# Kernel tuning notes

Hardware: AMD Instinct MI355X
Metric: run time of the kernel (lower is better)

Reference implementation:

```python
import jax, jax.numpy as jnp
import numpy as np

NUM_ITERATIONS = 5
BIG = 1e30


def _compute_cv(vc, Hf, norm):
    # vc: [B, M, N]; Hf: [M, N] float 0/1 mask; norm: scalar normalization factor
    # sign part: product of signs of incoming messages per check, redistributed
    sign_info = (1.0 - Hf)[None] + vc            # non-edges -> +1 so they don't affect the product
    s = jnp.sign(sign_info)
    row_sign = jnp.prod(s, axis=2, keepdims=True)  # [B, M, 1]
    result_sign = row_sign * Hf * s              # extrinsic sign per edge (self sign divided out)
    # magnitude part: min / second-min over edges of each check (masked top-2)
    back = jnp.where(Hf == 0.0, -BIG - 1.0, 0.0)[None]  # push non-edges to -inf-ish
    a = jnp.clip(jnp.abs(vc), 0.0, BIG)
    decision = -a + back                          # top-2 of this = two smallest magnitudes on edges
    top2 = jax.lax.top_k(decision, 2)[0]          # [B, M, 2]
    mn = (-top2[:, :, 0:1]) * Hf                  # smallest magnitude, broadcast on edges
    sub = (-top2[:, :, 1:2]) * Hf                 # second smallest
    res = jnp.where(a > mn, mn, sub)              # extrinsic min (exclude self if self is the min)
    return norm * res * jax.lax.stop_gradient(result_sign)


def setup_inputs() -> dict:
    key = jax.random.key(0)
    k1, k2, k3 = jax.random.split(key, 3)
    B, M, N = 16, 1024, 2048
    soft_input = jax.random.normal(k1, (B, N), dtype=jnp.float32) * 2.0
    # sparse binary parity-check matrix (Tanner graph), ~20 ones per row, min degree 2
    H = (jax.random.uniform(k2, (M, N)) < 0.01).astype(jnp.int32)
    H = H.at[:, :2].set(1)
    labels = jax.random.randint(k3, (B, N), 0, 2).astype(jnp.int32)
    w = jnp.full((1,), -0.048, dtype=jnp.float32)
    return {"soft_input": soft_input, "H": H, "labels": labels, "w": w}


def reference(soft_input, H, labels, w):
    Hf = H.astype(jnp.float32)
    norm = jax.nn.softplus(w)  # NMS-1 normalized factor, shape [1]
    soft_output = soft_input
    for _ in range(NUM_ITERATIONS):
        vc = soft_output[:, None, :] * Hf          # variable-to-check messages [B, M, N]
        cv = _compute_cv(vc, Hf, norm)             # check-to-variable messages [B, M, N]
        soft_output = soft_input + jnp.sum(cv, axis=1)  # marginalize
    return soft_output
```

## Files before the change

kernel.cpp:

```cpp
#include <hip/hip_runtime.h>

#define BB 16
#define MM 1024
#define NN 2048
#define RCAP 64
#define CCAP 48
#define NBLK 256
#define NTHR 1024
#define GRP  16
#define CPB  (NN / GRP)
#define INFF __builtin_inff()

typedef unsigned short u16;

__device__ __forceinline__ float signf(float x) {
    return (x > 0.0f) ? 1.0f : ((x < 0.0f) ? -1.0f : 0.0f);
}

__device__ __forceinline__ float loadB(const float* p) {
    unsigned u = __hip_atomic_load((const unsigned*)p, __ATOMIC_RELAXED,
                                   __HIP_MEMORY_SCOPE_AGENT);
    return __uint_as_float(u);
}
__device__ __forceinline__ void storeB(float* p, float v) {
    __hip_atomic_store((unsigned*)p, __float_as_uint(v), __ATOMIC_RELAXED,
                       __HIP_MEMORY_SCOPE_AGENT);
}

__device__ __forceinline__ void bar_global(int* c) {
    asm volatile("s_waitcnt vmcnt(0)" ::: "memory");
    __syncthreads();
    if (threadIdx.x == 0) {
        __hip_atomic_fetch_add(c, 1, __ATOMIC_ACQ_REL, __HIP_MEMORY_SCOPE_AGENT);
        while (__hip_atomic_load(c, __ATOMIC_RELAXED, __HIP_MEMORY_SCOPE_AGENT) < NBLK)
            __builtin_amdgcn_s_sleep(1);
        (void)__hip_atomic_load(c, __ATOMIC_ACQUIRE, __HIP_MEMORY_SCOPE_AGENT);
    }
    __syncthreads();
}

__device__ __forceinline__ void bar_group(int* c) {
    asm volatile("s_waitcnt vmcnt(0)" ::: "memory");
    __syncthreads();
    if (threadIdx.x == 0) {
        __hip_atomic_fetch_add(c, 1, __ATOMIC_RELAXED, __HIP_MEMORY_SCOPE_AGENT);
        while (__hip_atomic_load(c, __ATOMIC_RELAXED, __HIP_MEMORY_SCOPE_AGENT) < GRP)
            __builtin_amdgcn_s_sleep(1);
    }
    __syncthreads();
}

__global__ __launch_bounds__(NTHR)
void bp_one(const int4* __restrict__ H4, const float* __restrict__ soft_in,
            const float* __restrict__ wptr,
            int* __restrict__ ctrG, int* __restrict__ ctr2,
            int* __restrict__ col_deg, int* __restrict__ row_deg,
            u16* __restrict__ row_cols, u16* __restrict__ col_rows,
            float* __restrict__ sX, float* __restrict__ sY,
            float* __restrict__ out)
{
    __shared__ float  s_soft[NN];
    __shared__ float4 s_stats[MM];
    __shared__ u16    s_deg[MM];
    __shared__ u16    s_cols[4][RCAP];
    __shared__ int    s_cnt[4];

    const int t = threadIdx.x;

    if (t < 4) s_cnt[t] = 0;
    __syncthreads();
    const int lr = t >> 8;
    const int tt = t & 255;
    const int mrow = blockIdx.x * 4 + lr;
    {
        const int4* hrow = H4 + mrow * (NN / 4);
#pragma unroll
        for (int h = 0; h < 2; ++h) {
            int i = tt + (h << 8);
            int4 hv4 = hrow[i];
            int hv[4] = {hv4.x, hv4.y, hv4.z, hv4.w};
#pragma unroll
            for (int kk = 0; kk < 4; ++kk) {
                if (hv[kk]) {
                    int j = atomicAdd(&s_cnt[lr], 1);
                    if (j < RCAP) s_cols[lr][j] = (u16)(i * 4 + kk);
                }
            }
        }
    }
    __syncthreads();
    const int rdeg_local = min(s_cnt[lr], RCAP);
    if (tt == 0) row_deg[mrow] = rdeg_local;
    if (tt < 8) ((int4*)(row_cols + mrow * RCAP))[tt] = ((const int4*)s_cols[lr])[tt];
    if (tt < rdeg_local) {
        int c = s_cols[lr][tt];
        if (c >= 2) {
            int pos = atomicAdd(&col_deg[c], 1);
            if (pos < CCAP) col_rows[c * CCAP + pos] = (u16)mrow;
        }
    }
    bar_global(ctrG);

    const int g    = blockIdx.x & 15;
    const int rank = blockIdx.x >> 4;
    const float norm = log1pf(expf(wptr[0]));
    const float* sInG = soft_in + g * NN;
    float* sXg = sX + g * NN;
    float* sYg = sY + g * NN;
    float* outG = out + g * NN;

    s_deg[t] = (u16)row_deg[t];

    const int myCol = rank * CPB + (t >> 3);
    const int ll = t & 7;
    const int cdeg = (myCol >= 2) ? min(col_deg[myCol], CCAP) : 0;
    const bool cact = (ll < 6) && ((ll << 3) < cdeg);
    int4 ci = make_int4(0, 0, 0, 0);
    if (cact) ci = ((const int4*)(col_rows + myCol * CCAP))[ll];
    const float x_in_col = sInG[myCol];
    const bool heavy = (rank == 0) && (t < 128);
    const int hc = t >> 6;
    const float x_in_h = heavy ? sInG[hc] : 0.0f;
    __syncthreads();

#pragma unroll 1
    for (int it = 0; it < 5; ++it) {
        const float* curG = (it & 1) ? sXg : sYg;
        float* nxtG = (it & 1) ? sYg : sXg;

        {
            float v0, v1;
            if (it == 0) { v0 = sInG[t]; v1 = sInG[t + 1024]; }
            else         { v0 = loadB(curG + t); v1 = loadB(curG + t + 1024); }
            s_soft[t] = v0; s_soft[t + 1024] = v1;
        }
        __syncthreads();

        {
            const int deg = s_deg[t];
            const int4* ip = (const int4*)(row_cols + t * RCAP);
            float sgn = 1.0f, mn = INFF, sub = INFF;
#pragma unroll
            for (int jb = 0; jb < RCAP; jb += 8) {
                if (jb < deg) {
                    int4 iv = ip[jb >> 3];
                    const u16* q = (const u16*)&iv;
#pragma unroll
                    for (int k = 0; k < 8; ++k) {
                        float x = s_soft[q[k] & (NN - 1)];
                        x = (jb + k < deg) ? x : INFF;
                        sgn *= signf(x);
                        float a = fabsf(x);
                        if (a < mn) { sub = mn; mn = a; }
                        else if (a < sub) sub = a;
                    }
                }
            }
            s_stats[t] = make_float4(norm * sgn, mn, sub, 0.0f);
        }
        __syncthreads();

        float res;
        {
            float x = s_soft[myCol];
            float a = fabsf(x), sx = signf(x), acc = 0.0f;
            if (cact) {
                const u16* q = (const u16*)&ci;
                const int base = ll << 3;
#pragma unroll
                for (int k = 0; k < 8; ++k) {
                    float4 s = s_stats[q[k] & (MM - 1)];
                    float cv = s.x * ((a > s.y) ? s.y : s.z) * sx;
                    acc += (base + k < cdeg) ? cv : 0.0f;
                }
            }
            acc += __shfl_xor(acc, 1);
            acc += __shfl_xor(acc, 2);
            acc += __shfl_xor(acc, 4);
            res = x_in_col + acc;
        }
        float hres = 0.0f;
        if (heavy) {
            const int lane = t & 63;
            float x = s_soft[hc];
            float a = fabsf(x), sx = signf(x), acc = 0.0f;
#pragma unroll
            for (int i2 = 0; i2 < 16; ++i2) {
                float4 s = s_stats[lane + (i2 << 6)];
                acc += s.x * ((a > s.y) ? s.y : s.z) * sx;
            }
#pragma unroll
            for (int off = 1; off < 64; off <<= 1) acc += __shfl_xor(acc, off);
            hres = x_in_h + acc;
        }

        const bool writer = (ll == 0) && (myCol >= 2);
        const bool hwriter = heavy && ((t & 63) == 0);
        if (it < 4) {
            if (writer)  storeB(nxtG + myCol, res);
            if (hwriter) storeB(nxtG + hc, hres);
            bar_group(ctr2 + ((g << 2) + it) * 64);
        } else {
            if (writer)  outG[myCol] = res;
            if (hwriter) outG[hc] = hres;
        }
    }
}

extern "C" void kernel_launch(void* const* d_in, const int* in_sizes, int n_in,
                              void* d_out, int out_size, void* d_ws, size_t ws_size,
                              hipStream_t stream)
{
    const float* soft_in = (const float*)d_in[0];
    const int4*  H4      = (const int4*)d_in[1];
    const float* w       = (const float*)d_in[3];
    float* out = (float*)d_out;

    char* ws = (char*)d_ws;
    int* ctrG     = (int*)ws;
    int* ctr2     = (int*)(ws + 1024);
    int* col_deg  = (int*)(ws + 20480);
    int* row_deg  = (int*)(ws + 28672);
    u16* row_cols = (u16*)(ws + 32768);
    u16* col_rows = (u16*)(ws + 163840);
    float* sX     = (float*)(ws + 360448);
    float* sY     = (float*)(ws + 491520);

    hipMemsetAsync(ws, 0, 28672, stream);

    void* args[12] = { (void*)&H4, (void*)&soft_in, (void*)&w,
                       (void*)&ctrG, (void*)&ctr2, (void*)&col_deg,
                       (void*)&row_deg, (void*)&row_cols, (void*)&col_rows,
                       (void*)&sX, (void*)&sY, (void*)&out };
    hipLaunchCooperativeKernel((void*)bp_one, dim3(NBLK), dim3(NTHR),
                               args, 0, stream);
}
```

Before: 147.7 us.

## Replace counter barriers with flag barriers and vectorize inter-block exchange

```diff
diff --git a/kernel.cpp b/kernel.cpp
--- a/kernel.cpp
+++ b/kernel.cpp
@@ -12,66 +12,91 @@
 #define INFF __builtin_inff()
 
 typedef unsigned short u16;
+typedef unsigned int u32;
+typedef float f32x4 __attribute__((ext_vector_type(4)));
 
 __device__ __forceinline__ float signf(float x) {
     return (x > 0.0f) ? 1.0f : ((x < 0.0f) ? -1.0f : 0.0f);
 }
 
-__device__ __forceinline__ float loadB(const float* p) {
-    unsigned u = __hip_atomic_load((const unsigned*)p, __ATOMIC_RELAXED,
-                                   __HIP_MEMORY_SCOPE_AGENT);
-    return __uint_as_float(u);
-}
-__device__ __forceinline__ void storeB(float* p, float v) {
-    __hip_atomic_store((unsigned*)p, __float_as_uint(v), __ATOMIC_RELAXED,
-                       __HIP_MEMORY_SCOPE_AGENT);
-}
-
-__device__ __forceinline__ void bar_global(int* c) {
+__device__ __forceinline__ f32x4 loadB4(const float* p) {
+    f32x4 v;
+    asm volatile("global_load_dwordx4 %0, %1, off sc0 sc1\n\t"
+                 "s_waitcnt vmcnt(0)"
+                 : "=&v"(v) : "v"(p) : "memory");
+    return v;
+}
+__device__ __forceinline__ void storeB4(float* p, f32x4 v) {
+    asm volatile("global_store_dwordx4 %0, %1, off sc0 sc1"
+                 :: "v"(p), "v"(v) : "memory");
+}
+__device__ __forceinline__ int loadBi(const int* p) {
+    return __hip_atomic_load(p, __ATOMIC_RELAXED, __HIP_MEMORY_SCOPE_AGENT);
+}
+
+__device__ __forceinline__ void bar_build(int* bf) {
     asm volatile("s_waitcnt vmcnt(0)" ::: "memory");
     __syncthreads();
-    if (threadIdx.x == 0) {
-        __hip_atomic_fetch_add(c, 1, __ATOMIC_ACQ_REL, __HIP_MEMORY_SCOPE_AGENT);
-        while (__hip_atomic_load(c, __ATOMIC_RELAXED, __HIP_MEMORY_SCOPE_AGENT) < NBLK)
-            __builtin_amdgcn_s_sleep(1);
-        (void)__hip_atomic_load(c, __ATOMIC_ACQUIRE, __HIP_MEMORY_SCOPE_AGENT);
-    }
-    __syncthreads();
-}
-
-__device__ __forceinline__ void bar_group(int* c) {
+    if (threadIdx.x == 0)
+        __hip_atomic_store(bf + blockIdx.x, 1, __ATOMIC_RELEASE,
+                           __HIP_MEMORY_SCOPE_AGENT);
+    if (threadIdx.x < 64) {
+        const int i = (int)threadIdx.x << 2;
+        for (;;) {
+            int a = loadBi(bf + i) & loadBi(bf + i + 1) &
+                    loadBi(bf + i + 2) & loadBi(bf + i + 3);
+            if (__all(a)) break;
+            __builtin_amdgcn_s_sleep(8);
+        }
+    }
+    __syncthreads();
+    if (threadIdx.x == 0)
+        (void)__hip_atomic_load(bf, __ATOMIC_ACQUIRE, __HIP_MEMORY_SCOPE_AGENT);
+    __syncthreads();
+}
+
+__device__ __forceinline__ void bar_group(int* gf, int rank, int target) {
     asm volatile("s_waitcnt vmcnt(0)" ::: "memory");
     __syncthreads();
-    if (threadIdx.x == 0) {
-        __hip_atomic_fetch_add(c, 1, __ATOMIC_RELAXED, __HIP_MEMORY_SCOPE_AGENT);
-        while (__hip_atomic_load(c, __ATOMIC_RELAXED, __HIP_MEMORY_SCOPE_AGENT) < GRP)
-            __builtin_amdgcn_s_sleep(1);
-    }
-    __syncthreads();
-}
-
-__global__ __launch_bounds__(NTHR)
+    if (threadIdx.x == 0)
+        __hip_atomic_store(gf + rank, target, __ATOMIC_RELAXED,
+                           __HIP_MEMORY_SCOPE_AGENT);
+    if (threadIdx.x < 64) {
+        int v = 0x7fffffff;
+        for (;;) {
+            if (threadIdx.x < GRP) v = loadBi(gf + threadIdx.x);
+            if (__all(v >= target)) break;
+            __builtin_amdgcn_s_sleep(2);
+        }
+    }
+    __syncthreads();
+}
+
+__global__ __launch_bounds__(NTHR, 4)
 void bp_one(const int4* __restrict__ H4, const float* __restrict__ soft_in,
             const float* __restrict__ wptr,
-            int* __restrict__ ctrG, int* __restrict__ ctr2,
+            int* __restrict__ bflags, int* __restrict__ gflags,
             int* __restrict__ col_deg, int* __restrict__ row_deg,
             u16* __restrict__ row_cols, u16* __restrict__ col_rows,
             float* __restrict__ sX, float* __restrict__ sY,
             float* __restrict__ out)
 {
-    __shared__ float  s_soft[NN];
+    __shared__ float  s_soft[NN + 4];
     __shared__ float4 s_stats[MM];
-    __shared__ u16    s_deg[MM];
+    __shared__ float  s_res[CPB];
     __shared__ u16    s_cols[4][RCAP];
     __shared__ int    s_cnt[4];
 
     const int t = threadIdx.x;
 
     if (t < 4) s_cnt[t] = 0;
-    __syncthreads();
-    const int lr = t >> 8;
-    const int tt = t & 255;
-    const int mrow = blockIdx.x * 4 + lr;
+    {
+        const int lr0 = t >> 8, tt0 = t & 255;
+        if (tt0 < RCAP) s_cols[lr0][tt0] = (u16)NN;
+    }
+    __syncthreads();
+    const int lr = t >> 8, tt = t & 255;
+    const int mrow = (blockIdx.x << 2) + lr;
     {
         const int4* hrow = H4 + mrow * (NN / 4);
 #pragma unroll
@@ -89,27 +114,35 @@
         }
     }
     __syncthreads();
-    const int rdeg_local = min(s_cnt[lr], RCAP);
-    if (tt == 0) row_deg[mrow] = rdeg_local;
+    const int rdeg_l = min(s_cnt[lr], RCAP);
+    if (tt == 0) row_deg[mrow] = rdeg_l;
     if (tt < 8) ((int4*)(row_cols + mrow * RCAP))[tt] = ((const int4*)s_cols[lr])[tt];
-    if (tt < rdeg_local) {
+    if (tt < rdeg_l) {
         int c = s_cols[lr][tt];
         if (c >= 2) {
             int pos = atomicAdd(&col_deg[c], 1);
             if (pos < CCAP) col_rows[c * CCAP + pos] = (u16)mrow;
         }
     }
-    bar_global(ctrG);
+    bar_build(bflags);
 
     const int g    = blockIdx.x & 15;
     const int rank = blockIdx.x >> 4;
     const float norm = log1pf(expf(wptr[0]));
+    const u32 nbits = __float_as_uint(norm);
     const float* sInG = soft_in + g * NN;
     float* sXg = sX + g * NN;
     float* sYg = sY + g * NN;
     float* outG = out + g * NN;
-
-    s_deg[t] = (u16)row_deg[t];
+    int* gf = gflags + (g << 6);
+
+    const int rdeg = row_deg[t];
+    int4 ri[8];
+    {
+        const int4* p = (const int4*)(row_cols + t * RCAP);
+#pragma unroll
+        for (int j = 0; j < 8; ++j) ri[j] = p[j];
+    }
 
     const int myCol = rank * CPB + (t >> 3);
     const int ll = t & 7;
@@ -121,46 +154,45 @@
     const bool heavy = (rank == 0) && (t < 128);
     const int hc = t >> 6;
     const float x_in_h = heavy ? sInG[hc] : 0.0f;
-    __syncthreads();
+    if (t == 0) s_soft[NN] = INFF;
 
 #pragma unroll 1
     for (int it = 0; it < 5; ++it) {
         const float* curG = (it & 1) ? sXg : sYg;
         float* nxtG = (it & 1) ? sYg : sXg;
 
+        if (t < NN / 4) {
+            f32x4 v;
+            if (it == 0) v = ((const f32x4*)sInG)[t];
+            else         v = loadB4(curG + (t << 2));
+            ((f32x4*)s_soft)[t] = v;
+        }
+        __syncthreads();
+
         {
-            float v0, v1;
-            if (it == 0) { v0 = sInG[t]; v1 = sInG[t + 1024]; }
-            else         { v0 = loadB(curG + t); v1 = loadB(curG + t + 1024); }
-            s_soft[t] = v0; s_soft[t + 1024] = v1;
+            u32 sbits = 0;
+            float mn = INFF, sub = INFF;
+#pragma unroll
+            for (int jb = 0; jb < 8; ++jb) {
+                if ((jb << 3) < rdeg) {
+                    const int4 iv = ri[jb];
+                    const u32 w0 = (u32)iv.x, w1 = (u32)iv.y;
+                    const u32 w2 = (u32)iv.z, w3 = (u32)iv.w;
+#define PROC(c) { float x = s_soft[(c)]; sbits ^= __float_as_uint(x);      \
+                  float a = fabsf(x); float hi = fmaxf(mn, a);             \
+                  mn = fminf(mn, a); sub = fminf(sub, hi); }
+                    PROC(w0 & 0xffffu); PROC(w0 >> 16);
+                    PROC(w1 & 0xffffu); PROC(w1 >> 16);
+                    PROC(w2 & 0xffffu); PROC(w2 >> 16);
+                    PROC(w3 & 0xffffu); PROC(w3 >> 16);
+#undef PROC
+                }
+            }
+            s_stats[t] = make_float4(
+                __uint_as_float((sbits & 0x80000000u) | nbits), mn, sub, 0.0f);
         }
         __syncthreads();
 
-        {
-            const int deg = s_deg[t];
-            const int4* ip = (const int4*)(row_cols + t * RCAP);
-            float sgn = 1.0f, mn = INFF, sub = INFF;
-#pragma unroll
-            for (int jb = 0; jb < RCAP; jb += 8) {
-                if (jb < deg) {
-                    int4 iv = ip[jb >> 3];
-                    const u16* q = (const u16*)&iv;
-#pragma unroll
-                    for (int k = 0; k < 8; ++k) {
-                        float x = s_soft[q[k] & (NN - 1)];
-                        x = (jb + k < deg) ? x : INFF;
-                        sgn *= signf(x);
-                        float a = fabsf(x);
-                        if (a < mn) { sub = mn; mn = a; }
-                        else if (a < sub) sub = a;
-                    }
-                }
-            }
-            s_stats[t] = make_float4(norm * sgn, mn, sub, 0.0f);
-        }
-        __syncthreads();
-
-        float res;
         {
             float x = s_soft[myCol];
             float a = fabsf(x), sx = signf(x), acc = 0.0f;
@@ -177,9 +209,8 @@
             acc += __shfl_xor(acc, 1);
             acc += __shfl_xor(acc, 2);
             acc += __shfl_xor(acc, 4);
-            res = x_in_col + acc;
-        }
-        float hres = 0.0f;
+            if (ll == 0 && myCol >= 2) s_res[t >> 3] = x_in_col + acc;
+        }
         if (heavy) {
             const int lane = t & 63;
             float x = s_soft[hc];
@@ -191,18 +222,17 @@
             }
 #pragma unroll
             for (int off = 1; off < 64; off <<= 1) acc += __shfl_xor(acc, off);
-            hres = x_in_h + acc;
-        }
-
-        const bool writer = (ll == 0) && (myCol >= 2);
-        const bool hwriter = heavy && ((t & 63) == 0);
+            if (lane == 0) s_res[hc] = x_in_h + acc;
+        }
+        __syncthreads();
+
         if (it < 4) {
-            if (writer)  storeB(nxtG + myCol, res);
-            if (hwriter) storeB(nxtG + hc, hres);
-            bar_group(ctr2 + ((g << 2) + it) * 64);
+            if (t < CPB / 4)
+                storeB4(nxtG + rank * CPB + (t << 2), ((const f32x4*)s_res)[t]);
+            bar_group(gf, rank, it + 1);
         } else {
-            if (writer)  outG[myCol] = res;
-            if (hwriter) outG[hc] = hres;
+            if (t < CPB / 4)
+                ((float4*)(outG + rank * CPB))[t] = ((const float4*)s_res)[t];
         }
     }
 }
@@ -217,21 +247,21 @@
     float* out = (float*)d_out;
 
     char* ws = (char*)d_ws;
-    int* ctrG     = (int*)ws;
-    int* ctr2     = (int*)(ws + 1024);
-    int* col_deg  = (int*)(ws + 20480);
-    int* row_deg  = (int*)(ws + 28672);
-    u16* row_cols = (u16*)(ws + 32768);
-    u16* col_rows = (u16*)(ws + 163840);
-    float* sX     = (float*)(ws + 360448);
-    float* sY     = (float*)(ws + 491520);
-
-    hipMemsetAsync(ws, 0, 28672, stream);
+    int* bflags   = (int*)ws;
+    int* gflags   = (int*)(ws + 1024);
+    int* col_deg  = (int*)(ws + 8192);
+    int* row_deg  = (int*)(ws + 16384);
+    u16* row_cols = (u16*)(ws + 20480);
+    u16* col_rows = (u16*)(ws + 151552);
+    float* sX     = (float*)(ws + 348160);
+    float* sY     = (float*)(ws + 479232);
+
+    (void)hipMemsetAsync(ws, 0, 16384, stream);
 
     void* args[12] = { (void*)&H4, (void*)&soft_in, (void*)&w,
-                       (void*)&ctrG, (void*)&ctr2, (void*)&col_deg,
+                       (void*)&bflags, (void*)&gflags, (void*)&col_deg,
                        (void*)&row_deg, (void*)&row_cols, (void*)&col_rows,
                        (void*)&sX, (void*)&sY, (void*)&out };
-    hipLaunchCooperativeKernel((void*)bp_one, dim3(NBLK), dim3(NTHR),
-                               args, 0, stream);
-}
+    (void)hipLaunchCooperativeKernel((void*)bp_one, dim3(NBLK), dim3(NTHR),
+                                     args, 0, stream);
+}
```

Measured after the change: 132.9 us. 1.11x faster.
